# Optimization experiments

Hardware: AMD Instinct MI355X
Metric: run time of the kernel (lower is better)

Reference implementation:

```python
import jax, jax.numpy as jnp
import numpy as np

B, L, D = 8, 512, 512
VOCAB = 50257
N_CLASSES = 225          # ceil(sqrt(50257))
N_PER_CLASS = 224        # ceil(50257 / 225)


def _glorot(key, shape, fan_in, fan_out):
    s = np.sqrt(6.0 / (fan_in + fan_out)).astype(np.float32)
    return jax.random.uniform(key, shape, jnp.float32, -s, s)


def setup_inputs() -> dict:
    key = jax.random.key(0)
    k = jax.random.split(key, 4)
    x = jax.random.normal(k[0], (B, L, D), jnp.float32)
    target = jax.random.randint(k[1], (B, L), 0, VOCAB)
    W1 = _glorot(k[2], (D, N_CLASSES), D, N_CLASSES)
    b1 = jnp.zeros((N_CLASSES,), jnp.float32)
    W2 = _glorot(k[3], (N_CLASSES, D, N_PER_CLASS), D, N_PER_CLASS)
    b2 = jnp.zeros((N_CLASSES, N_PER_CLASS), jnp.float32)
    return {"x": x, "target": target, "W1": W1, "b1": b1, "W2": W2, "b2": b2}


def reference(x, target, W1, b1, W2, b2):
    # Theano h_softmax with target given: returns p(target | x), shape [B, L, 1].
    xf = x.reshape(-1, D)                      # [N, D]
    t = target.reshape(-1)                     # [N]
    cls = t // N_PER_CLASS                     # class id per token
    idx = t % N_PER_CLASS                      # within-class id per token

    class_p = jax.nn.softmax(xf @ W1 + b1, axis=-1)          # [N, C]

    W2g = W2[cls]                                            # gather: [N, D, O]
    in_logits = jnp.einsum('nd,ndo->no', xf, W2g) + b2[cls]  # [N, O]
    in_p = jax.nn.softmax(in_logits, axis=-1)                # [N, O]

    n = jnp.arange(xf.shape[0])
    p = class_p[n, cls] * in_p[n, idx]                       # [N]
    return p.reshape(B, L, 1)
```

## Files before the change

kernel.cpp:

```cpp
#include <hip/hip_runtime.h>
#include <cmath>

typedef _Float16 half8 __attribute__((ext_vector_type(8)));
typedef float f32x4 __attribute__((ext_vector_type(4)));

constexpr int D   = 512;
constexpr int NC  = 225;
constexpr int NPC = 224;
constexpr int N1  = 256;
constexpr int TB  = 32;

constexpr int WS_NCHUNK = 0;
constexpr int WS_CHUNK  = 16;
constexpr int WS_ORDER  = 4096;
constexpr int WS_B1P    = 8192;
constexpr int WS_W1H    = 8448;
constexpr int WS_W1L    = 73984;
constexpr int WS_XH     = 139520;
constexpr int WS_XL     = 1188096;
constexpr int WS_STAT   = 2236672;

__device__ __forceinline__ void f16split(float v, _Float16& h, _Float16& l) {
    _Float16 hh = (_Float16)v;
    float hf = (float)hh;
    if (fabsf(hf) < 6.104e-5f) { hh = (_Float16)0.f; hf = 0.f; }
    h = hh;
    l = (_Float16)((v - hf) * 2048.0f);
}

__global__ __launch_bounds__(256) void k_prep_pre(
    const float* __restrict__ x, const float* __restrict__ W1,
    const float* __restrict__ b1, const int* __restrict__ target,
    int* __restrict__ ws, int ntok)
{
    const int bid = blockIdx.x, tid = threadIdx.x;
    if (bid == 0) {
        __shared__ int h[256], sc[256], sc2[256], cur[NC];
        h[tid] = 0;
        __syncthreads();
        for (int n = tid; n < ntok; n += 256) atomicAdd(&h[target[n] / NPC], 1);
        __syncthreads();
        const int hv = h[tid];
        sc[tid] = hv; __syncthreads();
        for (int o = 1; o < 256; o <<= 1) {
            int a = (tid >= o) ? sc[tid - o] : 0;
            __syncthreads();
            sc[tid] += a;
            __syncthreads();
        }
        const int start = sc[tid] - hv;
        const int nch = (tid < NC) ? (hv + TB - 1) / TB : 0;
        sc2[tid] = nch; __syncthreads();
        for (int o = 1; o < 256; o <<= 1) {
            int a = (tid >= o) ? sc2[tid - o] : 0;
            __syncthreads();
            sc2[tid] += a;
            __syncthreads();
        }
        const int nch2 = sc2[255];
        if (tid < NC) {
            cur[tid] = start;
            const int cb = sc2[tid] - nch;
            for (int j = 0; j < nch; ++j) {
                for (int q = 0; q < 2; ++q) {
                    const int e = WS_CHUNK + (((cb + j) * 2) + q) * 4;
                    ws[e + 0] = tid;
                    ws[e + 1] = start + j * TB;
                    ws[e + 2] = min(TB, hv - j * TB);
                    ws[e + 3] = q;
                }
            }
        }
        const int P1C = ntok / TB;
        if (tid < P1C) {
            for (int q = 0; q < 2; ++q) {
                const int e = WS_CHUNK + (nch2 * 2 + tid * 2 + q) * 4;
                ws[e + 0] = -1;
                ws[e + 1] = tid * TB;
                ws[e + 2] = TB;
                ws[e + 3] = q;
            }
        }
        if (tid == 0) ws[WS_NCHUNK] = nch2 * 2 + P1C * 2;
        __syncthreads();
        for (int n = tid; n < ntok; n += 256) {
            const int c = target[n] / NPC;
            const int pos = atomicAdd(&cur[c], 1);
            ws[WS_ORDER + pos] = n;
        }
        return;
    }
    const int pb = bid - 1;
    _Float16* xh  = (_Float16*)(ws + WS_XH);
    _Float16* xl  = (_Float16*)(ws + WS_XL);
    _Float16* w1h = (_Float16*)(ws + WS_W1H);
    _Float16* w1l = (_Float16*)(ws + WS_W1L);
    const int XBLK = (ntok * D) / (256 * 8);
    if (pb < XBLK) {
        const int base = (pb * 256 + tid) * 8;
        const float4 a = *(const float4*)(x + base);
        const float4 b = *(const float4*)(x + base + 4);
        const float v[8] = {a.x, a.y, a.z, a.w, b.x, b.y, b.z, b.w};
        half8 hv, lv;
        #pragma unroll
        for (int j = 0; j < 8; ++j) {
            _Float16 hq, lq;
            f16split(v[j], hq, lq);
            hv[j] = hq; lv[j] = lq;
        }
        *(half8*)(xh + base) = hv;
        *(half8*)(xl + base) = lv;
    } else if (pb < XBLK + 64) {
        const int oi = ((pb - XBLK) * 256 + tid) * 8;
        const int c = oi >> 9, k0 = oi & 511;
        half8 hv, lv;
        #pragma unroll
        for (int j = 0; j < 8; ++j) {
            const float v = (c < NC) ? W1[(size_t)(k0 + j) * NC + c] : 0.f;
            _Float16 hq, lq;
            f16split(v, hq, lq);
            hv[j] = hq; lv[j] = lq;
        }
        *(half8*)(w1h + oi) = hv;
        *(half8*)(w1l + oi) = lv;
    } else {
        float* b1p = (float*)ws + WS_B1P;
        if (tid < N1) b1p[tid] = (tid < NC) ? b1[tid] : 0.f;
    }
}

template <bool PH2>
__device__ __forceinline__ void run_chunk(
    const int* __restrict__ target, const float* __restrict__ W2c,
    const float* __restrict__ bsrc,
    const _Float16* __restrict__ w1h, const _Float16* __restrict__ w1l,
    const _Float16* __restrict__ xh_g, const _Float16* __restrict__ xl_g,
    int* __restrict__ ws, int* __restrict__ stok,
    float* __restrict__ wtile, _Float16* __restrict__ xtile,
    int start, int cnt, int ch)
{
    constexpr int NREAL = PH2 ? NPC : NC;
    const int tid = threadIdx.x, w = tid >> 6, lane = tid & 63;
    const int l15 = lane & 15, l4 = lane >> 4;

    if (tid < TB)
        stok[tid] = PH2 ? ws[WS_ORDER + start + min(tid, cnt - 1)] : (start + tid);
    __syncthreads();

    const int ntiles = PH2 ? ((cnt + 15) >> 4) : 2;
    const int mt0 = PH2 ? (w * 2) : (ch * 8 + w * 2);
    bool tval[2];
    if (PH2) { tval[0] = (mt0 < 7); tval[1] = (mt0 + 1 < 7); }
    else     { tval[0] = (mt0 * 16) < NREAL; tval[1] = ((mt0 + 1) * 16) < NREAL; }

    const int part = w >> 1, halfsel = w & 1;
    const int xtok = stok[halfsel * 16 + (lane >> 2)];
    const size_t xsrcoff = (size_t)xtok * 1024 + (size_t)(lane & 3) * 16;
    const char* xsrc = part ? (const char*)xl_g : (const char*)xh_g;
    const char* gW = PH2 ? ((const char*)W2c + ch * 448) : nullptr;

    #define STAGE_X(buf, kt)                                                        \
        __builtin_amdgcn_global_load_lds(                                           \
            (const __attribute__((address_space(1))) uint32_t*)                     \
                (xsrc + xsrcoff + (size_t)(kt) * 64),                               \
            (__attribute__((address_space(3))) uint32_t*)                           \
                ((char*)xtile + (buf) * 4096 + part * 2048 + halfsel * 1024),       \
            16, 0, 0)

    #define STAGE_W(buf, kt)                                                        \
        do {                                                                        \
            const char* gb_ = gW + (size_t)(kt) * 28672;                            \
            _Pragma("unroll")                                                       \
            for (int i_ = 0; i_ < 4; ++i_) {                                        \
                const int ii_ = w + i_ * 4;                                         \
                if (ii_ < 14) {                                                     \
                    const int flat_ = ii_ * 1024 + lane * 16;                       \
                    const int row_ = flat_ / 448, off_ = flat_ % 448;               \
                    __builtin_amdgcn_global_load_lds(                               \
                        (const __attribute__((address_space(1))) uint32_t*)         \
                            (gb_ + (size_t)row_ * 896 + off_),                      \
                        (__attribute__((address_space(3))) uint32_t*)               \
                            (wtile + (buf) * 3584 + ii_ * 256),                     \
                        16, 0, 0);                                                  \
                }                                                                   \
            }                                                                       \
        } while (0)

    f32x4 accA[2][2] = {}, accB[2][2] = {};

    if (PH2) STAGE_W(0, 0);
    STAGE_X(0, 0);
    __syncthreads();

    for (int kt = 0; kt < 16; ++kt) {
        const int cur = kt & 1;
        if (kt + 1 < 16) {
            if (PH2) STAGE_W(cur ^ 1, kt + 1);
            STAGE_X(cur ^ 1, kt + 1);
        }
        const char* xb = (const char*)xtile + cur * 4096;
        half8 Bh[2], Bl[2];
        #pragma unroll
        for (int n = 0; n < 2; ++n) if (n < ntiles) {
            Bh[n] = *(const half8*)(xb + (n * 16 + l15) * 64 + l4 * 16);
            Bl[n] = *(const half8*)(xb + 2048 + (n * 16 + l15) * 64 + l4 * 16);
        }
        #pragma unroll
        for (int mi = 0; mi < 2; ++mi) if (tval[mi]) {
            half8 Ah, Al;
            if (PH2) {
                const float* wrow = wtile + cur * 3584 + (mt0 + mi) * 16 + l15;
                #pragma unroll
                for (int j = 0; j < 8; ++j) {
                    _Float16 hq, lq;
                    f16split(wrow[(l4 * 8 + j) * 112], hq, lq);
                    Ah[j] = hq; Al[j] = lq;
                }
            } else {
                const int col = (mt0 + mi) * 16 + l15;
                const int k0 = kt * 32;
                Ah = *(const half8*)(w1h + (size_t)col * D + k0 + l4 * 8);
                Al = *(const half8*)(w1l + (size_t)col * D + k0 + l4 * 8);
            }
            #pragma unroll
            for (int n = 0; n < 2; ++n) if (n < ntiles) {
                accA[mi][n] = __builtin_amdgcn_mfma_f32_16x16x32_f16(Ah, Bh[n], accA[mi][n], 0, 0, 0);
                accB[mi][n] = __builtin_amdgcn_mfma_f32_16x16x32_f16(Ah, Bl[n], accB[mi][n], 0, 0, 0);
                accB[mi][n] = __builtin_amdgcn_mfma_f32_16x16x32_f16(Al, Bh[n], accB[mi][n], 0, 0, 0);
            }
        }
        __syncthreads();
    }
    #undef STAGE_W
    #undef STAGE_X

    float* stat = (float*)ws + WS_STAT;
    #pragma unroll
    for (int n = 0; n < 2; ++n) {
        if (n < ntiles) {
            const int tok = stok[n * 16 + l15];
            const int tt  = target[tok];
            const int tcol = PH2 ? (tt % NPC) : (tt / NPC);
            float vals[2][4];
            float mx = -1e30f;
            #pragma unroll
            for (int mi = 0; mi < 2; ++mi) if (tval[mi]) {
                const int col0 = PH2 ? ((ch * 7 + mt0 + mi) * 16 + l4 * 4)
                                     : ((mt0 + mi) * 16 + l4 * 4);
                const float4 bv = *(const float4*)(bsrc + col0);
                #pragma unroll
                for (int r = 0; r < 4; ++r) {
                    const float v = accA[mi][n][r] + accB[mi][n][r] * (1.f / 2048.f) + (&bv.x)[r];
                    vals[mi][r] = v;
                    if (col0 + r < NREAL) mx = fmaxf(mx, v);
                }
            }
            mx = fmaxf(mx, __shfl_xor(mx, 16, 64));
            mx = fmaxf(mx, __shfl_xor(mx, 32, 64));
            float s = 0.f, e = 0.f;
            #pragma unroll
            for (int mi = 0; mi < 2; ++mi) if (tval[mi]) {
                const int col0 = PH2 ? ((ch * 7 + mt0 + mi) * 16 + l4 * 4)
                                     : ((mt0 + mi) * 16 + l4 * 4);
                #pragma unroll
                for (int r = 0; r < 4; ++r) {
                    const int cr = col0 + r;
                    if (cr < NREAL) {
                        const float ex = __expf(vals[mi][r] - mx);
                        s += ex;
                        if (cr == tcol) e = ex;
                    }
                }
            }
            s += __shfl_xor(s, 16, 64); s += __shfl_xor(s, 32, 64);
            e += __shfl_xor(e, 16, 64); e += __shfl_xor(e, 32, 64);
            if (l4 == 0) {
                const int g = (PH2 ? 8 : 0) + ch * 4 + w;
                *(float4*)(stat + (size_t)tok * 64 + g * 4) = {mx, s, e, 0.f};
            }
        }
    }
}

__global__ __launch_bounds__(256, 4) void k_main(
    const int* __restrict__ target, const float* __restrict__ W2,
    const float* __restrict__ b2, int* __restrict__ ws)
{
    __shared__ float wtile[2 * 3584];
    __shared__ _Float16 xtile[2 * 2048];
    __shared__ int stok[TB];
    const int bid = blockIdx.x;
    if (bid >= ws[WS_NCHUNK]) return;
    const int4 ce = *(const int4*)(ws + WS_CHUNK + bid * 4);
    const _Float16* w1h = (const _Float16*)(ws + WS_W1H);
    const _Float16* w1l = (const _Float16*)(ws + WS_W1L);
    const _Float16* xh  = (const _Float16*)(ws + WS_XH);
    const _Float16* xl  = (const _Float16*)(ws + WS_XL);
    if (ce.x >= 0) {
        run_chunk<true>(target, W2 + (size_t)ce.x * D * NPC, b2 + ce.x * NPC,
                        w1h, w1l, xh, xl, ws, stok, wtile, xtile, ce.y, ce.z, ce.w);
    } else {
        run_chunk<false>(target, nullptr, (const float*)ws + WS_B1P,
                         w1h, w1l, xh, xl, ws, stok, wtile, xtile, ce.y, ce.z, ce.w);
    }
}

__global__ __launch_bounds__(256) void k_combine(const int* __restrict__ ws,
                                                 float* __restrict__ out, int ntok) {
    const int n = blockIdx.x * 256 + threadIdx.x;
    if (n >= ntok) return;
    const float4* st = (const float4*)((const float*)ws + WS_STAT) + (size_t)n * 16;
    float p[2];
    #pragma unroll
    for (int ph = 0; ph < 2; ++ph) {
        float M = -1e30f;
        #pragma unroll
        for (int g = 0; g < 8; ++g) M = fmaxf(M, st[ph * 8 + g].x);
        float S = 0.f, E = 0.f;
        #pragma unroll
        for (int g = 0; g < 8; ++g) {
            const float4 q = st[ph * 8 + g];
            const float sc = __expf(q.x - M);
            S += q.y * sc;
            E += q.z * sc;
        }
        p[ph] = E / S;
    }
    out[n] = p[0] * p[1];
}

extern "C" void kernel_launch(void* const* d_in, const int* in_sizes, int n_in,
                              void* d_out, int out_size, void* d_ws, size_t ws_size,
                              hipStream_t stream) {
    const float* x      = (const float*)d_in[0];
    const int*   target = (const int*)  d_in[1];
    const float* W1     = (const float*)d_in[2];
    const float* b1     = (const float*)d_in[3];
    const float* W2     = (const float*)d_in[4];
    const float* b2     = (const float*)d_in[5];
    float* out = (float*)d_out;
    int*   wsi = (int*)d_ws;

    const int ntok = in_sizes[1];
    const int maxgrid = 2 * (NC + ntok / TB) + 2 * (ntok / TB);
    const int pregrid = 1 + (ntok * D) / (256 * 8) + 64 + 1;

    k_prep_pre<<<pregrid, 256, 0, stream>>>(x, W1, b1, target, wsi, ntok);
    k_main    <<<maxgrid, 256, 0, stream>>>(target, W2, b2, wsi);
    k_combine <<<(ntok + 255) / 256, 256, 0, stream>>>(wsi, out, ntok);
}
```

Before: 47.98 us.

## Deepen PH2 prefetch to two tiles ahead with manual vmcnt waits

In the phase-2 GEMM path the kernel now issues LDS loads for the next two k-tiles up front. It waits with explicit s_waitcnt vmcnt counts and raw s_barrier instead of __syncthreads, so an async load stays in flight while the current tile computes. The vmcnt thresholds depend on how many loads each wave issues (w<2 issues one more). This is meant to hide global-to-LDS latency. It risks correctness if the counts are wrong, and the hand-written waits and barriers are fragile.

```diff
diff --git a/kernel.cpp b/kernel.cpp
--- a/kernel.cpp
+++ b/kernel.cpp
@@ -186,53 +186,77 @@
             }                                                                       \
         } while (0)
 
+    #define COMPUTE_TILE(cur, kt)                                                   \
+        do {                                                                        \
+            const char* xb = (const char*)xtile + (cur) * 4096;                     \
+            half8 Bh[2], Bl[2];                                                     \
+            _Pragma("unroll")                                                       \
+            for (int n = 0; n < 2; ++n) if (n < ntiles) {                           \
+                Bh[n] = *(const half8*)(xb + (n * 16 + l15) * 64 + l4 * 16);        \
+                Bl[n] = *(const half8*)(xb + 2048 + (n * 16 + l15) * 64 + l4 * 16); \
+            }                                                                       \
+            _Pragma("unroll")                                                       \
+            for (int mi = 0; mi < 2; ++mi) if (tval[mi]) {                          \
+                half8 Ah, Al;                                                       \
+                if (PH2) {                                                          \
+                    const float* wrow = wtile + (cur) * 3584 + (mt0 + mi) * 16 + l15; \
+                    _Pragma("unroll")                                               \
+                    for (int j = 0; j < 8; ++j) {                                   \
+                        _Float16 hq, lq;                                            \
+                        f16split(wrow[(l4 * 8 + j) * 112], hq, lq);                 \
+                        Ah[j] = hq; Al[j] = lq;                                     \
+                    }                                                               \
+                } else {                                                            \
+                    const int col = (mt0 + mi) * 16 + l15;                          \
+                    const int k0 = (kt) * 32;                                       \
+                    Ah = *(const half8*)(w1h + (size_t)col * D + k0 + l4 * 8);      \
+                    Al = *(const half8*)(w1l + (size_t)col * D + k0 + l4 * 8);      \
+                }                                                                   \
+                _Pragma("unroll")                                                   \
+                for (int n = 0; n < 2; ++n) if (n < ntiles) {                       \
+                    accA[mi][n] = __builtin_amdgcn_mfma_f32_16x16x32_f16(Ah, Bh[n], accA[mi][n], 0, 0, 0); \
+                    accB[mi][n] = __builtin_amdgcn_mfma_f32_16x16x32_f16(Ah, Bl[n], accB[mi][n], 0, 0, 0); \
+                    accB[mi][n] = __builtin_amdgcn_mfma_f32_16x16x32_f16(Al, Bh[n], accB[mi][n], 0, 0, 0); \
+                }                                                                   \
+            }                                                                       \
+        } while (0)
+
     f32x4 accA[2][2] = {}, accB[2][2] = {};
 
-    if (PH2) STAGE_W(0, 0);
-    STAGE_X(0, 0);
-    __syncthreads();
-
-    for (int kt = 0; kt < 16; ++kt) {
-        const int cur = kt & 1;
-        if (kt + 1 < 16) {
-            if (PH2) STAGE_W(cur ^ 1, kt + 1);
-            STAGE_X(cur ^ 1, kt + 1);
-        }
-        const char* xb = (const char*)xtile + cur * 4096;
-        half8 Bh[2], Bl[2];
-        #pragma unroll
-        for (int n = 0; n < 2; ++n) if (n < ntiles) {
-            Bh[n] = *(const half8*)(xb + (n * 16 + l15) * 64 + l4 * 16);
-            Bl[n] = *(const half8*)(xb + 2048 + (n * 16 + l15) * 64 + l4 * 16);
-        }
-        #pragma unroll
-        for (int mi = 0; mi < 2; ++mi) if (tval[mi]) {
-            half8 Ah, Al;
-            if (PH2) {
-                const float* wrow = wtile + cur * 3584 + (mt0 + mi) * 16 + l15;
-                #pragma unroll
-                for (int j = 0; j < 8; ++j) {
-                    _Float16 hq, lq;
-                    f16split(wrow[(l4 * 8 + j) * 112], hq, lq);
-                    Ah[j] = hq; Al[j] = lq;
-                }
+    if constexpr (PH2) {
+        STAGE_W(0, 0); STAGE_X(0, 0);
+        STAGE_W(1, 1); STAGE_X(1, 1);
+        for (int kt = 0; kt < 16; ++kt) {
+            const int cur = kt & 1;
+            if (kt < 15) {
+                if (w < 2) asm volatile("s_waitcnt vmcnt(5)" ::: "memory");
+                else       asm volatile("s_waitcnt vmcnt(4)" ::: "memory");
             } else {
-                const int col = (mt0 + mi) * 16 + l15;
-                const int k0 = kt * 32;
-                Ah = *(const half8*)(w1h + (size_t)col * D + k0 + l4 * 8);
-                Al = *(const half8*)(w1l + (size_t)col * D + k0 + l4 * 8);
-            }
-            #pragma unroll
-            for (int n = 0; n < 2; ++n) if (n < ntiles) {
-                accA[mi][n] = __builtin_amdgcn_mfma_f32_16x16x32_f16(Ah, Bh[n], accA[mi][n], 0, 0, 0);
-                accB[mi][n] = __builtin_amdgcn_mfma_f32_16x16x32_f16(Ah, Bl[n], accB[mi][n], 0, 0, 0);
-                accB[mi][n] = __builtin_amdgcn_mfma_f32_16x16x32_f16(Al, Bh[n], accB[mi][n], 0, 0, 0);
-            }
-        }
+                asm volatile("s_waitcnt vmcnt(0)" ::: "memory");
+            }
+            __builtin_amdgcn_sched_barrier(0);
+            __builtin_amdgcn_s_barrier();
+            __builtin_amdgcn_sched_barrier(0);
+
+            COMPUTE_TILE(cur, kt);
+
+            __builtin_amdgcn_s_barrier();
+            __builtin_amdgcn_sched_barrier(0);
+            if (kt + 2 < 16) { STAGE_W(cur, kt + 2); STAGE_X(cur, kt + 2); }
+        }
+    } else {
+        STAGE_X(0, 0);
         __syncthreads();
+        for (int kt = 0; kt < 16; ++kt) {
+            const int cur = kt & 1;
+            if (kt + 1 < 16) STAGE_X(cur ^ 1, kt + 1);
+            COMPUTE_TILE(cur, kt);
+            __syncthreads();
+        }
     }
     #undef STAGE_W
     #undef STAGE_X
+    #undef COMPUTE_TILE
 
     float* stat = (float*)ws + WS_STAT;
     #pragma unroll
```

After: 48.36 us. Within noise of the previous version (+0.8%).

## Split phase-2 chunks into quarters with swizzled LDS and a deeper load pipeline

Applied to the files above, without the earlier changes.

Each phase-2 class chunk is now split into four column quarters of 56 outputs instead of two halves, which doubles the number of phase-2 blocks and halves the W2 tile each block stages. The W2 LDS tile uses an XOR swizzle to cut bank conflicts, and staging becomes a two-stage-ahead prefetch synchronised with explicit vmcnt waits and raw barriers. The templated chunk routine is split into separate phase-1 and phase-2 routines, occupancy is raised to 5 blocks, and the stat layout and combine kernel now handle 24 partial groups. In exchange it adds more blocks and more combine work, and the hand-written waitcnt counts are fragile if the number of loads per wave changes.

```diff
diff --git a/kernel.cpp b/kernel.cpp
--- a/kernel.cpp
+++ b/kernel.cpp
@@ -12,13 +12,13 @@
 
 constexpr int WS_NCHUNK = 0;
 constexpr int WS_CHUNK  = 16;
-constexpr int WS_ORDER  = 4096;
-constexpr int WS_B1P    = 8192;
-constexpr int WS_W1H    = 8448;
-constexpr int WS_W1L    = 73984;
-constexpr int WS_XH     = 139520;
-constexpr int WS_XL     = 1188096;
-constexpr int WS_STAT   = 2236672;
+constexpr int WS_ORDER  = 8192;
+constexpr int WS_B1P    = 12288;
+constexpr int WS_W1H    = 12544;
+constexpr int WS_W1L    = 78080;
+constexpr int WS_XH     = 143616;
+constexpr int WS_XL     = 1192192;
+constexpr int WS_STAT   = 2240768;
 
 __device__ __forceinline__ void f16split(float v, _Float16& h, _Float16& l) {
     _Float16 hh = (_Float16)v;
@@ -27,6 +27,8 @@
     h = hh;
     l = (_Float16)((v - hf) * 2048.0f);
 }
+
+__device__ __forceinline__ int swz(int b) { return b ^ (((b >> 8) & 3) << 6); }
 
 __global__ __launch_bounds__(256) void k_prep_pre(
     const float* __restrict__ x, const float* __restrict__ W1,
@@ -62,8 +64,8 @@
             cur[tid] = start;
             const int cb = sc2[tid] - nch;
             for (int j = 0; j < nch; ++j) {
-                for (int q = 0; q < 2; ++q) {
-                    const int e = WS_CHUNK + (((cb + j) * 2) + q) * 4;
+                for (int q = 0; q < 4; ++q) {
+                    const int e = WS_CHUNK + (((cb + j) * 4) + q) * 4;
                     ws[e + 0] = tid;
                     ws[e + 1] = start + j * TB;
                     ws[e + 2] = min(TB, hv - j * TB);
@@ -74,14 +76,14 @@
         const int P1C = ntok / TB;
         if (tid < P1C) {
             for (int q = 0; q < 2; ++q) {
-                const int e = WS_CHUNK + (nch2 * 2 + tid * 2 + q) * 4;
+                const int e = WS_CHUNK + (nch2 * 4 + tid * 2 + q) * 4;
                 ws[e + 0] = -1;
                 ws[e + 1] = tid * TB;
                 ws[e + 2] = TB;
                 ws[e + 3] = q;
             }
         }
-        if (tid == 0) ws[WS_NCHUNK] = nch2 * 2 + P1C * 2;
+        if (tid == 0) ws[WS_NCHUNK] = nch2 * 4 + P1C * 2;
         __syncthreads();
         for (int n = tid; n < ntok; n += 256) {
             const int c = target[n] / NPC;
@@ -129,35 +131,39 @@
     }
 }
 
-template <bool PH2>
-__device__ __forceinline__ void run_chunk(
+__device__ __forceinline__ void run_p2(
     const int* __restrict__ target, const float* __restrict__ W2c,
     const float* __restrict__ bsrc,
-    const _Float16* __restrict__ w1h, const _Float16* __restrict__ w1l,
     const _Float16* __restrict__ xh_g, const _Float16* __restrict__ xl_g,
     int* __restrict__ ws, int* __restrict__ stok,
     float* __restrict__ wtile, _Float16* __restrict__ xtile,
     int start, int cnt, int ch)
 {
-    constexpr int NREAL = PH2 ? NPC : NC;
     const int tid = threadIdx.x, w = tid >> 6, lane = tid & 63;
     const int l15 = lane & 15, l4 = lane >> 4;
 
-    if (tid < TB)
-        stok[tid] = PH2 ? ws[WS_ORDER + start + min(tid, cnt - 1)] : (start + tid);
+    if (tid < TB) stok[tid] = ws[WS_ORDER + start + min(tid, cnt - 1)];
     __syncthreads();
 
-    const int ntiles = PH2 ? ((cnt + 15) >> 4) : 2;
-    const int mt0 = PH2 ? (w * 2) : (ch * 8 + w * 2);
-    bool tval[2];
-    if (PH2) { tval[0] = (mt0 < 7); tval[1] = (mt0 + 1 < 7); }
-    else     { tval[0] = (mt0 * 16) < NREAL; tval[1] = ((mt0 + 1) * 16) < NREAL; }
+    const int ntiles = (cnt + 15) >> 4;
 
     const int part = w >> 1, halfsel = w & 1;
     const int xtok = stok[halfsel * 16 + (lane >> 2)];
     const size_t xsrcoff = (size_t)xtok * 1024 + (size_t)(lane & 3) * 16;
     const char* xsrc = part ? (const char*)xl_g : (const char*)xh_g;
-    const char* gW = PH2 ? ((const char*)W2c + ch * 448) : nullptr;
+    const char* gW = (const char*)W2c + ch * 224;
+
+    int rowi[2], offi[2];
+    #pragma unroll
+    for (int i = 0; i < 2; ++i) {
+        const int ii = w + 4 * i;
+        if (ii < 7) {
+            const int flat = ii * 1024 + lane * 16;
+            const int g = swz(flat);
+            rowi[i] = g / 224;
+            offi[i] = g % 224;
+        } else { rowi[i] = 0; offi[i] = 0; }
+    }
 
     #define STAGE_X(buf, kt)                                                        \
         __builtin_amdgcn_global_load_lds(                                           \
@@ -169,35 +175,38 @@
 
     #define STAGE_W(buf, kt)                                                        \
         do {                                                                        \
-            const char* gb_ = gW + (size_t)(kt) * 28672;                            \
             _Pragma("unroll")                                                       \
-            for (int i_ = 0; i_ < 4; ++i_) {                                        \
-                const int ii_ = w + i_ * 4;                                         \
-                if (ii_ < 14) {                                                     \
-                    const int flat_ = ii_ * 1024 + lane * 16;                       \
-                    const int row_ = flat_ / 448, off_ = flat_ % 448;               \
+            for (int i_ = 0; i_ < 2; ++i_) {                                        \
+                const int ii_ = w + 4 * i_;                                         \
+                if (ii_ < 7) {                                                      \
                     __builtin_amdgcn_global_load_lds(                               \
                         (const __attribute__((address_space(1))) uint32_t*)         \
-                            (gb_ + (size_t)row_ * 896 + off_),                      \
+                            (gW + (size_t)((kt) * 32 + rowi[i_]) * 896 + offi[i_]), \
                         (__attribute__((address_space(3))) uint32_t*)               \
-                            (wtile + (buf) * 3584 + ii_ * 256),                     \
+                            ((char*)wtile + (buf) * 7168 + ii_ * 1024),             \
                         16, 0, 0);                                                  \
                 }                                                                   \
             }                                                                       \
         } while (0)
 
-    f32x4 accA[2][2] = {}, accB[2][2] = {};
-
-    if (PH2) STAGE_W(0, 0);
-    STAGE_X(0, 0);
-    __syncthreads();
+    f32x4 accA[2] = {}, accB[2] = {};
+    const int qcolc = min(w * 16 + l15, 55);
+
+    STAGE_W(0, 0); STAGE_X(0, 0);
+    STAGE_W(1, 1); STAGE_X(1, 1);
 
     for (int kt = 0; kt < 16; ++kt) {
         const int cur = kt & 1;
-        if (kt + 1 < 16) {
-            if (PH2) STAGE_W(cur ^ 1, kt + 1);
-            STAGE_X(cur ^ 1, kt + 1);
-        }
+        if (kt < 15) {
+            if (w < 3) asm volatile("s_waitcnt vmcnt(3)" ::: "memory");
+            else       asm volatile("s_waitcnt vmcnt(2)" ::: "memory");
+        } else {
+            asm volatile("s_waitcnt vmcnt(0)" ::: "memory");
+        }
+        __builtin_amdgcn_sched_barrier(0);
+        __builtin_amdgcn_s_barrier();
+        __builtin_amdgcn_sched_barrier(0);
+
         const char* xb = (const char*)xtile + cur * 4096;
         half8 Bh[2], Bl[2];
         #pragma unroll
@@ -205,25 +214,120 @@
             Bh[n] = *(const half8*)(xb + (n * 16 + l15) * 64 + l4 * 16);
             Bl[n] = *(const half8*)(xb + 2048 + (n * 16 + l15) * 64 + l4 * 16);
         }
-        #pragma unroll
-        for (int mi = 0; mi < 2; ++mi) if (tval[mi]) {
-            half8 Ah, Al;
-            if (PH2) {
-                const float* wrow = wtile + cur * 3584 + (mt0 + mi) * 16 + l15;
-                #pragma unroll
-                for (int j = 0; j < 8; ++j) {
-                    _Float16 hq, lq;
-                    f16split(wrow[(l4 * 8 + j) * 112], hq, lq);
-                    Ah[j] = hq; Al[j] = lq;
+        half8 Ah, Al;
+        {
+            const char* wb = (const char*)wtile + cur * 7168;
+            #pragma unroll
+            for (int j = 0; j < 8; ++j) {
+                const int lin = (l4 * 8 + j) * 224 + qcolc * 4;
+                const float v = *(const float*)(wb + swz(lin));
+                _Float16 hq, lq;
+                f16split(v, hq, lq);
+                Ah[j] = hq; Al[j] = lq;
+            }
+        }
+        #pragma unroll
+        for (int n = 0; n < 2; ++n) if (n < ntiles) {
+            accA[n] = __builtin_amdgcn_mfma_f32_16x16x32_f16(Ah, Bh[n], accA[n], 0, 0, 0);
+            accB[n] = __builtin_amdgcn_mfma_f32_16x16x32_f16(Ah, Bl[n], accB[n], 0, 0, 0);
+            accB[n] = __builtin_amdgcn_mfma_f32_16x16x32_f16(Al, Bh[n], accB[n], 0, 0, 0);
+        }
+
+        __builtin_amdgcn_s_barrier();
+        __builtin_amdgcn_sched_barrier(0);
+        if (kt + 2 < 16) { STAGE_W(cur, kt + 2); STAGE_X(cur, kt + 2); }
+    }
+    #undef STAGE_W
+    #undef STAGE_X
+
+    float* stat = (float*)ws + WS_STAT;
+    const int qc0 = w * 16 + l4 * 4;
+    const float4 bv = *(const float4*)(bsrc + ch * 56 + min(qc0, 52));
+    #pragma unroll
+    for (int n = 0; n < 2; ++n) {
+        if (n < ntiles) {
+            const int tok = stok[n * 16 + l15];
+            const int tloc = (target[tok] % NPC) - ch * 56;
+            float vals[4];
+            float mx = -1e30f;
+            #pragma unroll
+            for (int r = 0; r < 4; ++r) {
+                const float v = accA[n][r] + accB[n][r] * (1.f / 2048.f) + (&bv.x)[r];
+                vals[r] = v;
+                if (qc0 + r < 56) mx = fmaxf(mx, v);
+            }
+            mx = fmaxf(mx, __shfl_xor(mx, 16, 64));
+            mx = fmaxf(mx, __shfl_xor(mx, 32, 64));
+            float s = 0.f, e = 0.f;
+            #pragma unroll
+            for (int r = 0; r < 4; ++r) {
+                const int qc = qc0 + r;
+                if (qc < 56) {
+                    const float ex = __expf(vals[r] - mx);
+                    s += ex;
+                    if (qc == tloc) e = ex;
                 }
-            } else {
-                const int col = (mt0 + mi) * 16 + l15;
-                const int k0 = kt * 32;
-                Ah = *(const half8*)(w1h + (size_t)col * D + k0 + l4 * 8);
-                Al = *(const half8*)(w1l + (size_t)col * D + k0 + l4 * 8);
-            }
-            #pragma unroll
-            for (int n = 0; n < 2; ++n) if (n < ntiles) {
+            }
+            s += __shfl_xor(s, 16, 64); s += __shfl_xor(s, 32, 64);
+            e += __shfl_xor(e, 16, 64); e += __shfl_xor(e, 32, 64);
+            if (l4 == 0) {
+                const int g = 8 + ch * 4 + w;
+                *(float4*)(stat + (size_t)tok * 128 + g * 4) = {mx, s, e, 0.f};
+            }
+        }
+    }
+}
+
+__device__ __forceinline__ void run_p1(
+    const int* __restrict__ target, const float* __restrict__ bsrc,
+    const _Float16* __restrict__ w1h, const _Float16* __restrict__ w1l,
+    const _Float16* __restrict__ xh_g, const _Float16* __restrict__ xl_g,
+    int* __restrict__ ws, int* __restrict__ stok, _Float16* __restrict__ xtile,
+    int start, int ch)
+{
+    constexpr int NREAL = NC;
+    const int tid = threadIdx.x, w = tid >> 6, lane = tid & 63;
+    const int l15 = lane & 15, l4 = lane >> 4;
+
+    if (tid < TB) stok[tid] = start + tid;
+    __syncthreads();
+
+    const int part = w >> 1, halfsel = w & 1;
+    const int xtok = stok[halfsel * 16 + (lane >> 2)];
+    const size_t xsrcoff = (size_t)xtok * 1024 + (size_t)(lane & 3) * 16;
+    const char* xsrc = part ? (const char*)xl_g : (const char*)xh_g;
+
+    #define STAGE_X(buf, kt)                                                        \
+        __builtin_amdgcn_global_load_lds(                                           \
+            (const __attribute__((address_space(1))) uint32_t*)                     \
+                (xsrc + xsrcoff + (size_t)(kt) * 64),                               \
+            (__attribute__((address_space(3))) uint32_t*)                           \
+                ((char*)xtile + (buf) * 4096 + part * 2048 + halfsel * 1024),       \
+            16, 0, 0)
+
+    const int mt0 = ch * 8 + w * 2;
+    f32x4 accA[2][2] = {}, accB[2][2] = {};
+
+    STAGE_X(0, 0);
+    __syncthreads();
+    for (int kt = 0; kt < 16; ++kt) {
+        const int cur = kt & 1;
+        if (kt + 1 < 16) STAGE_X(cur ^ 1, kt + 1);
+        const char* xb = (const char*)xtile + cur * 4096;
+        half8 Bh[2], Bl[2];
+        #pragma unroll
+        for (int n = 0; n < 2; ++n) {
+            Bh[n] = *(const half8*)(xb + (n * 16 + l15) * 64 + l4 * 16);
+            Bl[n] = *(const half8*)(xb + 2048 + (n * 16 + l15) * 64 + l4 * 16);
+        }
+        #pragma unroll
+        for (int mi = 0; mi < 2; ++mi) {
+            const int col = (mt0 + mi) * 16 + l15;
+            const int k0 = kt * 32;
+            const half8 Ah = *(const half8*)(w1h + (size_t)col * D + k0 + l4 * 8);
+            const half8 Al = *(const half8*)(w1l + (size_t)col * D + k0 + l4 * 8);
+            #pragma unroll
+            for (int n = 0; n < 2; ++n) {
                 accA[mi][n] = __builtin_amdgcn_mfma_f32_16x16x32_f16(Ah, Bh[n], accA[mi][n], 0, 0, 0);
                 accB[mi][n] = __builtin_amdgcn_mfma_f32_16x16x32_f16(Ah, Bl[n], accB[mi][n], 0, 0, 0);
                 accB[mi][n] = __builtin_amdgcn_mfma_f32_16x16x32_f16(Al, Bh[n], accB[mi][n], 0, 0, 0);
@@ -231,62 +335,56 @@
         }
         __syncthreads();
     }
-    #undef STAGE_W
     #undef STAGE_X
 
     float* stat = (float*)ws + WS_STAT;
     #pragma unroll
     for (int n = 0; n < 2; ++n) {
-        if (n < ntiles) {
-            const int tok = stok[n * 16 + l15];
-            const int tt  = target[tok];
-            const int tcol = PH2 ? (tt % NPC) : (tt / NPC);
-            float vals[2][4];
-            float mx = -1e30f;
-            #pragma unroll
-            for (int mi = 0; mi < 2; ++mi) if (tval[mi]) {
-                const int col0 = PH2 ? ((ch * 7 + mt0 + mi) * 16 + l4 * 4)
-                                     : ((mt0 + mi) * 16 + l4 * 4);
-                const float4 bv = *(const float4*)(bsrc + col0);
-                #pragma unroll
-                for (int r = 0; r < 4; ++r) {
-                    const float v = accA[mi][n][r] + accB[mi][n][r] * (1.f / 2048.f) + (&bv.x)[r];
-                    vals[mi][r] = v;
-                    if (col0 + r < NREAL) mx = fmaxf(mx, v);
+        const int tok = stok[n * 16 + l15];
+        const int tcol = target[tok] / NPC;
+        float vals[2][4];
+        float mx = -1e30f;
+        #pragma unroll
+        for (int mi = 0; mi < 2; ++mi) {
+            const int col0 = (mt0 + mi) * 16 + l4 * 4;
+            const float4 bv = *(const float4*)(bsrc + col0);
+            #pragma unroll
+            for (int r = 0; r < 4; ++r) {
+                const float v = accA[mi][n][r] + accB[mi][n][r] * (1.f / 2048.f) + (&bv.x)[r];
+                vals[mi][r] = v;
+                if (col0 + r < NREAL) mx = fmaxf(mx, v);
+            }
+        }
+        mx = fmaxf(mx, __shfl_xor(mx, 16, 64));
+        mx = fmaxf(mx, __shfl_xor(mx, 32, 64));
+        float s = 0.f, e = 0.f;
+        #pragma unroll
+        for (int mi = 0; mi < 2; ++mi) {
+            const int col0 = (mt0 + mi) * 16 + l4 * 4;
+            #pragma unroll
+            for (int r = 0; r < 4; ++r) {
+                const int cr = col0 + r;
+                if (cr < NREAL) {
+                    const float ex = __expf(vals[mi][r] - mx);
+                    s += ex;
+                    if (cr == tcol) e = ex;
                 }
             }
-            mx = fmaxf(mx, __shfl_xor(mx, 16, 64));
-            mx = fmaxf(mx, __shfl_xor(mx, 32, 64));
-            float s = 0.f, e = 0.f;
-            #pragma unroll
-            for (int mi = 0; mi < 2; ++mi) if (tval[mi]) {
-                const int col0 = PH2 ? ((ch * 7 + mt0 + mi) * 16 + l4 * 4)
-                                     : ((mt0 + mi) * 16 + l4 * 4);
-                #pragma unroll
-                for (int r = 0; r < 4; ++r) {
-                    const int cr = col0 + r;
-                    if (cr < NREAL) {
-                        const float ex = __expf(vals[mi][r] - mx);
-                        s += ex;
-                        if (cr == tcol) e = ex;
-                    }
-                }
-            }
-            s += __shfl_xor(s, 16, 64); s += __shfl_xor(s, 32, 64);
-            e += __shfl_xor(e, 16, 64); e += __shfl_xor(e, 32, 64);
-            if (l4 == 0) {
-                const int g = (PH2 ? 8 : 0) + ch * 4 + w;
-                *(float4*)(stat + (size_t)tok * 64 + g * 4) = {mx, s, e, 0.f};
-            }
-        }
-    }
-}
-
-__global__ __launch_bounds__(256, 4) void k_main(
+        }
+        s += __shfl_xor(s, 16, 64); s += __shfl_xor(s, 32, 64);
+        e += __shfl_xor(e, 16, 64); e += __shfl_xor(e, 32, 64);
+        if (l4 == 0) {
+            const int g = ch * 4 + w;
+            *(float4*)(stat + (size_t)tok * 128 + g * 4) = {mx, s, e, 0.f};
+        }
+    }
+}
+
+__global__ __launch_bounds__(256, 5) void k_main(
     const int* __restrict__ target, const float* __restrict__ W2,
     const float* __restrict__ b2, int* __restrict__ ws)
 {
-    __shared__ float wtile[2 * 3584];
+    __shared__ float wtile[2 * 1792];
     __shared__ _Float16 xtile[2 * 2048];
     __shared__ int stok[TB];
     const int bid = blockIdx.x;
@@ -297,11 +395,11 @@
     const _Float16* xh  = (const _Float16*)(ws + WS_XH);
     const _Float16* xl  = (const _Float16*)(ws + WS_XL);
     if (ce.x >= 0) {
-        run_chunk<true>(target, W2 + (size_t)ce.x * D * NPC, b2 + ce.x * NPC,
-                        w1h, w1l, xh, xl, ws, stok, wtile, xtile, ce.y, ce.z, ce.w);
+        run_p2(target, W2 + (size_t)ce.x * D * NPC, b2 + ce.x * NPC,
+               xh, xl, ws, stok, wtile, xtile, ce.y, ce.z, ce.w);
     } else {
-        run_chunk<false>(target, nullptr, (const float*)ws + WS_B1P,
-                         w1h, w1l, xh, xl, ws, stok, wtile, xtile, ce.y, ce.z, ce.w);
+        run_p1(target, (const float*)ws + WS_B1P, w1h, w1l,
+               xh, xl, ws, stok, xtile, ce.y, ce.w);
     }
 }
 
@@ -309,24 +407,26 @@
                                                  float* __restrict__ out, int ntok) {
     const int n = blockIdx.x * 256 + threadIdx.x;
     if (n >= ntok) return;
-    const float4* st = (const float4*)((const float*)ws + WS_STAT) + (size_t)n * 16;
-    float p[2];
-    #pragma unroll
-    for (int ph = 0; ph < 2; ++ph) {
-        float M = -1e30f;
-        #pragma unroll
-        for (int g = 0; g < 8; ++g) M = fmaxf(M, st[ph * 8 + g].x);
-        float S = 0.f, E = 0.f;
-        #pragma unroll
-        for (int g = 0; g < 8; ++g) {
-            const float4 q = st[ph * 8 + g];
-            const float sc = __expf(q.x - M);
-            S += q.y * sc;
-            E += q.z * sc;
-        }
-        p[ph] = E / S;
-    }
-    out[n] = p[0] * p[1];
+    const float4* st = (const float4*)((const float*)ws + WS_STAT) + (size_t)n * 32;
+    float M1 = -1e30f, M2 = -1e30f;
+    #pragma unroll
+    for (int g = 0; g < 8; ++g)  M1 = fmaxf(M1, st[g].x);
+    #pragma unroll
+    for (int g = 8; g < 24; ++g) M2 = fmaxf(M2, st[g].x);
+    float S1 = 0.f, E1 = 0.f, S2 = 0.f, E2 = 0.f;
+    #pragma unroll
+    for (int g = 0; g < 8; ++g) {
+        const float4 q = st[g];
+        const float sc = __expf(q.x - M1);
+        S1 += q.y * sc; E1 += q.z * sc;
+    }
+    #pragma unroll
+    for (int g = 8; g < 24; ++g) {
+        const float4 q = st[g];
+        const float sc = __expf(q.x - M2);
+        S2 += q.y * sc; E2 += q.z * sc;
+    }
+    out[n] = (E1 / S1) * (E2 / S2);
 }
 
 extern "C" void kernel_launch(void* const* d_in, const int* in_sizes, int n_in,
@@ -342,7 +442,7 @@
     int*   wsi = (int*)d_ws;
 
     const int ntok = in_sizes[1];
-    const int maxgrid = 2 * (NC + ntok / TB) + 2 * (ntok / TB);
+    const int maxgrid = 4 * (NC + ntok / TB) + 2 * (ntok / TB);
     const int pregrid = 1 + (ntok * D) / (256 * 8) + 64 + 1;
 
     k_prep_pre<<<pregrid, 256, 0, stream>>>(x, W1, b1, target, wsi, ntok);
```

Result: slower. 56.24 us (+17.2%).
